# Kernel tuning notes

Measured on AMD Instinct MI355X. Metric: run time of the kernel, lower is better.

The kernel has to match this reference:

```python
import jax, jax.numpy as jnp
import numpy as np

N_NODES = 100000
N_EDGES = 1000000
NFEAT = 64
NHID = 64
NCLASS = 10
DROPOUT = 0.3
PAE_HID = 128  # hidden width of PAE in HOGCN/EV-GCN
EPS_BN = 1e-5
EPS_COS = 1e-8


def setup_inputs() -> dict:
    key = jax.random.key(0)
    ks = jax.random.split(key, 16)
    def w(k, shape, fan_in):
        return jax.random.normal(k, shape, dtype=jnp.float32) * (1.0 / np.sqrt(fan_in))
    inp = {
        "x": jax.random.normal(ks[0], (N_NODES, NFEAT), dtype=jnp.float32),
        "edge_index": jax.random.randint(ks[1], (2, N_EDGES), 0, N_NODES, dtype=jnp.int32),
        "edgenet_input": jax.random.normal(ks[2], (N_EDGES, 4), dtype=jnp.float32),
        # PAE params: Linear(2,128) -> ReLU -> BN(128) -> Dropout -> Linear(128,128)
        "pae_w1": w(ks[3], (2, PAE_HID), 2),
        "pae_b1": jnp.zeros((PAE_HID,), jnp.float32),
        "pae_gamma": jnp.ones((PAE_HID,), jnp.float32),
        "pae_beta": jnp.zeros((PAE_HID,), jnp.float32),
        "pae_w2": w(ks[4], (PAE_HID, PAE_HID), PAE_HID),
        "pae_b2": jnp.zeros((PAE_HID,), jnp.float32),
        # GCNConv layers
        "conv1_w": w(ks[5], (NFEAT, NHID), NFEAT),
        "conv1_b": jnp.zeros((NHID,), jnp.float32),
        "conv2_w": w(ks[6], (NHID, NHID), NHID),
        "conv2_b": jnp.zeros((NHID,), jnp.float32),
        # MLP head
        "lin1_w": w(ks[7], (NHID, NHID // 2), NHID),
        "lin1_b": jnp.zeros((NHID // 2,), jnp.float32),
        "lin2_w": w(ks[8], (NHID // 2, NCLASS), NHID // 2),
        "lin2_b": jnp.zeros((NCLASS,), jnp.float32),
    }
    return inp


def _pae(edgenet_input, w1, b1, gamma, beta, w2, b2, key):
    # Split edge input into the two endpoint halves; run shared parser on both.
    d = edgenet_input.shape[1] // 2
    x12 = jnp.stack([edgenet_input[:, :d], edgenet_input[:, d:]], axis=0)  # [2, E, d]
    h = jax.nn.relu(x12 @ w1 + b1)  # [2, E, H]
    # BatchNorm1d (training mode): stats over the edge batch, per parser call
    mean = h.mean(axis=1, keepdims=True)
    var = h.var(axis=1, keepdims=True)
    h = (h - mean) * jax.lax.rsqrt(var + EPS_BN) * gamma + beta
    keep = jax.random.bernoulli(key, 1.0 - DROPOUT, h.shape)
    h = jnp.where(keep, h / (1.0 - DROPOUT), 0.0)
    h = h @ w2 + b2
    h1, h2 = h[0], h[1]
    n1 = jnp.maximum(jnp.linalg.norm(h1, axis=-1), EPS_COS)
    n2 = jnp.maximum(jnp.linalg.norm(h2, axis=-1), EPS_COS)
    cos = (h1 * h2).sum(-1) / (n1 * n2)
    return (cos + 1.0) * 0.5  # [E]


def _gcn_conv(x, row, col, ew, W, b, n):
    # PyG GCNConv: add self-loops (weight 1), symmetric normalization, then
    # gather-scale-scatter aggregation of linearly transformed features.
    xw = x @ W  # [N, out]
    sl = jnp.arange(n, dtype=row.dtype)
    row_f = jnp.concatenate([row, sl])
    col_f = jnp.concatenate([col, sl])
    ew_f = jnp.concatenate([ew, jnp.ones((n,), ew.dtype)])
    deg = jax.ops.segment_sum(ew_f, col_f, num_segments=n)
    dinv = jnp.where(deg > 0, jax.lax.rsqrt(jnp.maximum(deg, 1e-12)), 0.0)
    norm = dinv[row_f] * ew_f * dinv[col_f]  # [E+N]
    msgs = norm[:, None] * xw[row_f]  # irregular gather + scale
    out = jax.ops.segment_sum(msgs, col_f, num_segments=n)  # scatter-add
    return out + b


def reference(x, edge_index, edgenet_input,
              pae_w1, pae_b1, pae_gamma, pae_beta, pae_w2, pae_b2,
              conv1_w, conv1_b, conv2_w, conv2_b,
              lin1_w, lin1_b, lin2_w, lin2_b):
    n = x.shape[0]
    row, col = edge_index[0], edge_index[1]
    k_pae, k_head = jax.random.split(jax.random.key(42))
    edge_weight = _pae(edgenet_input, pae_w1, pae_b1, pae_gamma, pae_beta,
                       pae_w2, pae_b2, k_pae)
    h = jax.nn.relu(_gcn_conv(x, row, col, edge_weight, conv1_w, conv1_b, n))
    h = jax.nn.relu(_gcn_conv(h, row, col, edge_weight, conv2_w, conv2_b, n))
    h = jax.nn.relu(h @ lin1_w + lin1_b)
    keep = jax.random.bernoulli(k_head, 1.0 - DROPOUT, h.shape)
    h = jnp.where(keep, h / (1.0 - DROPOUT), 0.0)
    out = h @ lin2_w + lin2_b
    return out
```

## Files before the change

kernel.cpp:

```cpp
#include <hip/hip_runtime.h>
#include <stdint.h>


#define NN 100000
#define NE 1000000
#define INV_KEEP (1.0f/0.7f)
#define KEEP_THR 3006477312u

#define BN_BLOCKS   1000
#define HIST_BLOCKS 3907
#define PAE_BLOCKS  31250
#define XW1_BLOCKS  1563
#define MEGA_GROUPS 782
#define MEGA_BLOCKS (MEGA_GROUPS * 47)

typedef short bf16x8 __attribute__((ext_vector_type(8)));
typedef float f32x4  __attribute__((ext_vector_type(4)));
typedef uint32_t u32x4 __attribute__((ext_vector_type(4)));

__host__ __device__ constexpr uint32_t rotl32c(uint32_t x, int r) {
  return (x << r) | (x >> (32 - r));
}

struct TFK { uint32_t a, b; };
__host__ __device__ constexpr TFK tf_const(uint32_t k0, uint32_t k1,
                                           uint32_t x0, uint32_t x1) {
  uint32_t k2 = k0 ^ k1 ^ 0x1BD11BDAu;
  x0 += k0; x1 += k1;
#define TFC_R(r) { x0 += x1; x1 = rotl32c(x1, (r)); x1 ^= x0; }
  TFC_R(13) TFC_R(15) TFC_R(26) TFC_R(6)   x0 += k1; x1 += k2 + 1u;
  TFC_R(17) TFC_R(29) TFC_R(16) TFC_R(24)  x0 += k2; x1 += k0 + 2u;
  TFC_R(13) TFC_R(15) TFC_R(26) TFC_R(6)   x0 += k0; x1 += k1 + 3u;
  TFC_R(17) TFC_R(29) TFC_R(16) TFC_R(24)  x0 += k1; x1 += k2 + 4u;
  TFC_R(13) TFC_R(15) TFC_R(26) TFC_R(6)   x0 += k2; x1 += k0 + 5u;
#undef TFC_R
  return TFK{x0, x1};
}

constexpr TFK KP = tf_const(0u, 42u, 0u, 0u);
constexpr TFK KH = tf_const(0u, 42u, 0u, 1u);

template <uint32_t K0, uint32_t K1>
__device__ __forceinline__ uint32_t tf_bits(uint32_t idx) {
  constexpr uint32_t K2 = K0 ^ K1 ^ 0x1BD11BDAu;
  uint32_t x0 = K0;
  uint32_t x1 = idx + K1;
#define TF_R(r) { x0 += x1; \
    x1 = __builtin_amdgcn_alignbit(x1, x1, 32u - (r)) ^ x0; }
  TF_R(13) TF_R(15) TF_R(26) TF_R(6)   x0 += K1; x1 += K2 + 1u;
  TF_R(17) TF_R(29) TF_R(16) TF_R(24)  x0 += K2; x1 += K0 + 2u;
  TF_R(13) TF_R(15) TF_R(26) TF_R(6)   x0 += K0; x1 += K1 + 3u;
  TF_R(17) TF_R(29) TF_R(16) TF_R(24)  x0 += K1; x1 += K2 + 4u;
  TF_R(13) TF_R(15) TF_R(26) TF_R(6)   x0 += K2; x1 += K0 + 5u;
#undef TF_R
  return x0 ^ x1;
}

__device__ __forceinline__ uint16_t f2bf(float f) {
  uint32_t u = __float_as_uint(f);
  return (uint16_t)((u + 0x7FFFu + ((u >> 16) & 1u)) >> 16);
}

__device__ __forceinline__ float bf2f(uint16_t u) {
  return __uint_as_float((uint32_t)u << 16);
}

__global__ __launch_bounds__(256) void phase1(const float* __restrict__ edgenet,
                                              const float* __restrict__ w1,
                                              const float* __restrict__ b1,
                                              const int* __restrict__ colp,
                                              float* __restrict__ sums,
                                              int* __restrict__ cnt) {
  int b = blockIdx.x;
  int t = threadIdx.x;
  if (b < BN_BLOCKS) {
    int c = t & 127, g = t >> 7;
    float wA = w1[c], wB = w1[128 + c], bb = b1[c];
    const float4* ed4 = (const float4*)edgenet;
    int e0 = b * 1000;
    float s0 = 0.f, q0 = 0.f, s1 = 0.f, q1 = 0.f;
#pragma unroll 4
    for (int e = g; e < 1000; e += 2) {
      float4 x = ed4[e0 + e];
      float h = fmaxf(fmaf(x.y, wB, fmaf(x.x, wA, bb)), 0.f);
      s0 += h; q0 = fmaf(h, h, q0);
      h = fmaxf(fmaf(x.w, wB, fmaf(x.z, wA, bb)), 0.f);
      s1 += h; q1 = fmaf(h, h, q1);
    }
    atomicAdd(&sums[c], s0);
    atomicAdd(&sums[256 + c], q0);
    atomicAdd(&sums[128 + c], s1);
    atomicAdd(&sums[384 + c], q1);
  } else {
    int e = (b - BN_BLOCKS) * 256 + t;
    if (e < NE) atomicAdd(&cnt[colp[e]], 1);
  }
}

__global__ __launch_bounds__(256) void csr_scanA(const int* __restrict__ cnt,
                                                 int* __restrict__ ptr,
                                                 int* __restrict__ bsum) {
  __shared__ int sh[256];
  int t = threadIdx.x;
  int i = blockIdx.x * 256 + t;
  int x = (i < NN) ? cnt[i] : 0;
  sh[t] = x;
  __syncthreads();
  for (int o = 1; o < 256; o <<= 1) {
    int v = (t >= o) ? sh[t - o] : 0;
    __syncthreads();
    sh[t] += v;
    __syncthreads();
  }
  if (i < NN) ptr[i] = sh[t] - x;
  if (t == 255) bsum[blockIdx.x] = sh[255];
}

__global__ __launch_bounds__(512) void scanAddPrep(const int* __restrict__ bsum,
                                                   int* __restrict__ ptr,
                                                   int* __restrict__ fill,
                                                   const float* __restrict__ sums,
                                                   const float* __restrict__ w1,
                                                   const float* __restrict__ b1,
                                                   const float* __restrict__ gamma,
                                                   const float* __restrict__ beta,
                                                   const float* __restrict__ w2,
                                                   float* __restrict__ prm,
                                                   uint32_t* __restrict__ w2t) {
  int b = blockIdx.x;
  int t = threadIdx.x;
  if (b < 391) {
    __shared__ int sh[512];
    int x = (t < 391) ? bsum[t] : 0;
    sh[t] = x;
    __syncthreads();
    for (int o = 1; o < 512; o <<= 1) {
      int v = (t >= o) ? sh[t - o] : 0;
      __syncthreads();
      sh[t] += v;
      __syncthreads();
    }
    int excl = (b == 0) ? 0 : sh[b - 1];
    if (t < 256) {
      int i = b * 256 + t;
      if (i < NN) {
        int v = ptr[i] + excl;
        ptr[i] = v;
        fill[i] = v;
        if (i == NN - 1) ptr[NN] = NE;
      }
    }
  } else if (b < 407) {
    int i = (b - 391) * 512 + t;
    int n = i >> 6, kp = i & 63;
    float f0 = w2[(2 * kp) * 128 + n];
    float f1 = w2[(2 * kp + 1) * 128 + n];
    w2t[i] = (uint32_t)f2bf(f0) | ((uint32_t)f2bf(f1) << 16);
  } else if (t < 256) {
    int c = t & 127;
    const float invE = 1.0f / (float)NE;
    float mean = sums[t] * invE;
    float var = fmaxf(sums[256 + t] * invE - mean * mean, 0.f);
    float rstd = rsqrtf(var + 1e-5f);
    float a = gamma[c] * rstd;
    prm[384 + t] = a * INV_KEEP;
    prm[640 + t] = (beta[c] - mean * a) * INV_KEEP;
    if (t < 128) { prm[t] = w1[t]; prm[128 + t] = w1[128 + t]; prm[256 + t] = b1[t]; }
  }
}

__global__ __launch_bounds__(256, 6) void mega(const float* __restrict__ edgenet,
                                               const float* __restrict__ prm_g,
                                               const uint32_t* __restrict__ w2t,
                                               const float* __restrict__ b2,
                                               const int* __restrict__ rowp,
                                               const int* __restrict__ colp,
                                               float* __restrict__ ew_out,
                                               float* __restrict__ deg,
                                               int* __restrict__ fill,
                                               int2* __restrict__ epk,
                                               const float* __restrict__ x,
                                               const float* __restrict__ c1w,
                                               uint16_t* __restrict__ xw1) {
  __shared__ __align__(16) uint8_t smem[17408];
  int b = blockIdx.x;
  int t = threadIdx.x;
  int g = b % 47, u = b / 47;

  if (g < 40) {
    int blk = u * 40 + g;
    if (blk >= PAE_BLOCKS) return;
    float* prm = (float*)smem;
    float* b2s = (float*)(smem + 3584);
    int e0 = blk * 32;
    for (int i = t; i < 896; i += 256) prm[i] = prm_g[i];
    if (t < 128) b2s[t] = b2[t];
    __syncthreads();

    int lane = t & 63, w = t >> 6;
    int cl = lane & 15, quad = lane >> 4;
    int quad8 = quad * 8;
    int row = 16 * w + cl;
    int el = row >> 1, s = row & 1;
    int so = s << 7;
    float2 xv = *(const float2*)&edgenet[(size_t)(e0 + el) * 4 + 2 * s];
    uint32_t rowbase = (uint32_t)(e0 + el) * 128u + (s ? 128000000u : 0u);
    const u32x4* w2v = (const u32x4*)w2t;

    f32x4 acc[8];
#pragma unroll
    for (int nt = 0; nt < 8; ++nt) acc[nt] = (f32x4){0.f, 0.f, 0.f, 0.f};

#pragma unroll 1
    for (int kt = 0; kt < 4; ++kt) {
      u32x4 bfv[8];
#pragma unroll
      for (int nt = 0; nt < 8; ++nt)
        bfv[nt] = w2v[(nt * 16 + cl) * 16 + kt * 4 + quad];

      int c0 = kt * 32 + quad8;
      uint32_t idxbase = rowbase + (uint32_t)c0;
      float wa[8], wb[8], bb[8], ak[8], bk[8];
      *(float4*)&wa[0] = *(const float4*)&prm[c0];
      *(float4*)&wa[4] = *(const float4*)&prm[c0 + 4];
      *(float4*)&wb[0] = *(const float4*)&prm[128 + c0];
      *(float4*)&wb[4] = *(const float4*)&prm[132 + c0];
      *(float4*)&bb[0] = *(const float4*)&prm[256 + c0];
      *(float4*)&bb[4] = *(const float4*)&prm[260 + c0];
      *(float4*)&ak[0] = *(const float4*)&prm[384 + so + c0];
      *(float4*)&ak[4] = *(const float4*)&prm[388 + so + c0];
      *(float4*)&bk[0] = *(const float4*)&prm[640 + so + c0];
      *(float4*)&bk[4] = *(const float4*)&prm[644 + so + c0];
      uint32_t pk[4];
#pragma unroll
      for (int jp = 0; jp < 4; ++jp) {
        uint32_t uu[2];
#pragma unroll
        for (int q = 0; q < 2; ++q) {
          int j = 2 * jp + q;
          float h = fmaxf(fmaf(xv.y, wb[j], fmaf(xv.x, wa[j], bb[j])), 0.f);
          float hn = fmaf(h, ak[j], bk[j]);
          uint32_t bits = tf_bits<KP.a, KP.b>(idxbase + (uint32_t)j);
          float hd = (bits < KEEP_THR) ? hn : 0.f;
          uu[q] = __float_as_uint(hd) + 0x8000u;
        }
        pk[jp] = __builtin_amdgcn_perm(uu[1], uu[0], 0x07060302u);
      }
      u32x4 pkv = {pk[0], pk[1], pk[2], pk[3]};
      bf16x8 afr = __builtin_bit_cast(bf16x8, pkv);
#pragma unroll
      for (int nt = 0; nt < 8; ++nt) {
        bf16x8 bfr = __builtin_bit_cast(bf16x8, bfv[nt]);
        acc[nt] = __builtin_amdgcn_mfma_f32_16x16x32_bf16(afr, bfr, acc[nt], 0, 0, 0);
      }
    }

    float p11[2] = {0.f, 0.f}, p22[2] = {0.f, 0.f}, p12[2] = {0.f, 0.f};
#pragma unroll
    for (int nt = 0; nt < 8; ++nt) {
      float bv = b2s[nt * 16 + cl];
#pragma unroll
      for (int uq = 0; uq < 2; ++uq) {
        float v1 = acc[nt][2 * uq] + bv;
        float v2 = acc[nt][2 * uq + 1] + bv;
        p11[uq] = fmaf(v1, v1, p11[uq]);
        p22[uq] = fmaf(v2, v2, p22[uq]);
        p12[uq] = fmaf(v1, v2, p12[uq]);
      }
    }
#pragma unroll
    for (int uq = 0; uq < 2; ++uq) {
      float a = p11[uq], bq = p22[uq], d = p12[uq];
      for (int off = 1; off < 16; off <<= 1) {
        a += __shfl_xor(a, off, 64);
        bq += __shfl_xor(bq, off, 64);
        d += __shfl_xor(d, off, 64);
      }
      if (cl == 0) {
        int e = e0 + 8 * w + 2 * quad + uq;
        float n1 = fmaxf(sqrtf(a), 1e-8f);
        float n2 = fmaxf(sqrtf(bq), 1e-8f);
        float ew = (d / (n1 * n2) + 1.f) * 0.5f;
        ew_out[e] = ew;
        atomicAdd(&deg[colp[e]], ew);
      }
    }
  } else if (g < 45) {
    int blk = u * 5 + (g - 40);
    if (blk >= HIST_BLOCKS) return;
    int e = blk * 256 + t;
    if (e < NE) {
      int r = rowp[e];
      int p = atomicAdd(&fill[colp[e]], 1);
      epk[p] = make_int2(r, e);
    }
  } else {
    int blk = u * 2 + (g - 45);
    if (blk >= XW1_BLOCKS) return;
    float* InT = (float*)smem;
    int v0 = blk * 64;
    for (int i = t; i < 4096; i += 256) {
      int v = i >> 6, k = i & 63;
      int vv = min(v0 + v, NN - 1);
      InT[k * 68 + v] = x[(size_t)vv * 64 + k];
    }
    __syncthreads();
    int tx = t & 15, ty = t >> 4;
    float acc[4][4];
#pragma unroll
    for (int i = 0; i < 4; ++i)
#pragma unroll
      for (int j = 0; j < 4; ++j) acc[i][j] = 0.f;
#pragma unroll 4
    for (int k = 0; k < 64; ++k) {
      float4 av = *(const float4*)&InT[k * 68 + 4 * ty];
      float4 bv = *(const float4*)&c1w[k * 64 + 4 * tx];
      float a4[4] = {av.x, av.y, av.z, av.w};
      float b4[4] = {bv.x, bv.y, bv.z, bv.w};
#pragma unroll
      for (int i = 0; i < 4; ++i)
#pragma unroll
        for (int j = 0; j < 4; ++j) acc[i][j] = fmaf(a4[i], b4[j], acc[i][j]);
    }
    for (int i = 0; i < 4; ++i) {
      int v = v0 + 4 * ty + i;
      if (v < NN) {
        uint32_t p0 = __builtin_amdgcn_perm(__float_as_uint(acc[i][1]) + 0x8000u,
                                            __float_as_uint(acc[i][0]) + 0x8000u,
                                            0x07060302u);
        uint32_t p1 = __builtin_amdgcn_perm(__float_as_uint(acc[i][3]) + 0x8000u,
                                            __float_as_uint(acc[i][2]) + 0x8000u,
                                            0x07060302u);
        *(uint2*)&xw1[(size_t)v * 64 + 4 * tx] = make_uint2(p0, p1);
      }
    }
  }
}

__global__ void csr_coef(int2* __restrict__ epk, const float* __restrict__ ew,
                         const float* __restrict__ deg) {
  int p = (blockIdx.x * 256 + threadIdx.x) * 2;
  if (p < NE) {
    int2 a = epk[p];
    int2 b = epk[p + 1];
    float da = deg[a.x], db = deg[b.x];
    float ea = ew[a.y], eb = ew[b.y];
    epk[p]     = make_int2(a.x, __float_as_int(rsqrtf(da + 1.0f) * ea));
    epk[p + 1] = make_int2(b.x, __float_as_int(rsqrtf(db + 1.0f) * eb));
  }
}

__global__ __launch_bounds__(256) void conv1g(const int* __restrict__ ptr,
                                              const int2* __restrict__ epk,
                                              const float* __restrict__ deg,
                                              const uint16_t* __restrict__ xw,
                                              const float* __restrict__ bias,
                                              uint16_t* __restrict__ h1) {
  int t = threadIdx.x;
  int v = blockIdx.x * 4 + (t >> 6);
  int c = t & 63;
  int p = ptr[v], end = ptr[v + 1];
  float acc = 0.f;
  while (p + 4 <= end) {
    int2 e0 = epk[p], e1 = epk[p + 1], e2 = epk[p + 2], e3 = epk[p + 3];
    float x0 = bf2f(xw[(size_t)e0.x * 64 + c]);
    float x1 = bf2f(xw[(size_t)e1.x * 64 + c]);
    float x2 = bf2f(xw[(size_t)e2.x * 64 + c]);
    float x3 = bf2f(xw[(size_t)e3.x * 64 + c]);
    acc = fmaf(__int_as_float(e0.y), x0, acc);
    acc = fmaf(__int_as_float(e1.y), x1, acc);
    acc = fmaf(__int_as_float(e2.y), x2, acc);
    acc = fmaf(__int_as_float(e3.y), x3, acc);
    p += 4;
  }
  if (p + 2 <= end) {
    int2 e0 = epk[p], e1 = epk[p + 1];
    float x0 = bf2f(xw[(size_t)e0.x * 64 + c]);
    float x1 = bf2f(xw[(size_t)e1.x * 64 + c]);
    acc = fmaf(__int_as_float(e0.y), x0, acc);
    acc = fmaf(__int_as_float(e1.y), x1, acc);
    p += 2;
  }
  if (p < end) {
    int2 a = epk[p];
    acc = fmaf(__int_as_float(a.y), bf2f(xw[(size_t)a.x * 64 + c]), acc);
  }
  float dv = rsqrtf(deg[v] + 1.0f);
  float val = fmaf(dv, acc, fmaf(dv * dv, bf2f(xw[(size_t)v * 64 + c]), bias[c]));
  h1[(size_t)v * 64 + c] = f2bf(fmaxf(val, 0.f));
}

__global__ __launch_bounds__(256) void conv2_head(const int* __restrict__ ptr,
                                                  const int2* __restrict__ epk,
                                                  const float* __restrict__ deg,
                                                  const uint16_t* __restrict__ h1,
                                                  const float* __restrict__ W,
                                                  const float* __restrict__ bias,
                                                  const float* __restrict__ l1w,
                                                  const float* __restrict__ l1b,
                                                  const float* __restrict__ l2w,
                                                  const float* __restrict__ l2b,
                                                  float* __restrict__ out) {
  __shared__ __align__(16) float T[16 * 68];
  __shared__ __align__(16) float H2[16 * 68];
  __shared__ float L2s[320];
  __shared__ float biass[64], l1bs[32], l2bs[16];
  int t = threadIdx.x;
  for (int i = t; i < 320; i += 256) L2s[i] = l2w[i];
  if (t < 64) biass[t] = bias[t];
  if (t < 32) l1bs[t] = l1b[t];
  if (t < 10) l2bs[t] = l2b[t];
  int w = t >> 6, c = t & 63;
  int v0 = blockIdx.x * 16;
#pragma unroll 1
  for (int i = 0; i < 4; ++i) {
    int n = 4 * w + i;
    int v = v0 + n;
    int p = ptr[v], end = ptr[v + 1];
    float acc = 0.f;
    while (p + 4 <= end) {
      int2 e0 = epk[p], e1 = epk[p + 1], e2 = epk[p + 2], e3 = epk[p + 3];
      float x0 = bf2f(h1[(size_t)e0.x * 64 + c]);
      float x1 = bf2f(h1[(size_t)e1.x * 64 + c]);
      float x2 = bf2f(h1[(size_t)e2.x * 64 + c]);
      float x3 = bf2f(h1[(size_t)e3.x * 64 + c]);
      acc = fmaf(__int_as_float(e0.y), x0, acc);
      acc = fmaf(__int_as_float(e1.y), x1, acc);
      acc = fmaf(__int_as_float(e2.y), x2, acc);
      acc = fmaf(__int_as_float(e3.y), x3, acc);
      p += 4;
    }
    if (p + 2 <= end) {
      int2 e0 = epk[p], e1 = epk[p + 1];
      float x0 = bf2f(h1[(size_t)e0.x * 64 + c]);
      float x1 = bf2f(h1[(size_t)e1.x * 64 + c]);
      acc = fmaf(__int_as_float(e0.y), x0, acc);
      acc = fmaf(__int_as_float(e1.y), x1, acc);
      p += 2;
    }
    if (p < end) {
      int2 a = epk[p];
      acc = fmaf(__int_as_float(a.y), bf2f(h1[(size_t)a.x * 64 + c]), acc);
    }
    float dv = rsqrtf(deg[v] + 1.0f);
    T[n * 68 + c] = fmaf(dv, acc, dv * dv * bf2f(h1[(size_t)v * 64 + c]));
  }
  __syncthreads();
  {
    int n = t >> 4, cq = (t & 15) * 4;
    float4 o = *(const float4*)&biass[cq];
#pragma unroll 4
    for (int k = 0; k < 64; ++k) {
      float a = T[n * 68 + k];
      float4 wv = *(const float4*)&W[k * 64 + cq];
      o.x = fmaf(a, wv.x, o.x);
      o.y = fmaf(a, wv.y, o.y);
      o.z = fmaf(a, wv.z, o.z);
      o.w = fmaf(a, wv.w, o.w);
    }
    o.x = fmaxf(o.x, 0.f); o.y = fmaxf(o.y, 0.f);
    o.z = fmaxf(o.z, 0.f); o.w = fmaxf(o.w, 0.f);
    __syncthreads();
    *(float4*)&H2[n * 68 + cq] = o;
  }
  __syncthreads();
  {
    int n = t >> 4, j0 = t & 15;
#pragma unroll
    for (int jj = 0; jj < 2; ++jj) {
      int j = j0 + 16 * jj;
      float m = l1bs[j];
#pragma unroll 4
      for (int k = 0; k < 64; ++k) m = fmaf(H2[n * 68 + k], l1w[k * 32 + j], m);
      m = fmaxf(m, 0.f);
      uint32_t idx = (uint32_t)(v0 + n) * 32u + (uint32_t)j;
      bool kp = tf_bits<KH.a, KH.b>(idx) < KEEP_THR;
      T[n * 33 + j] = kp ? m * INV_KEEP : 0.f;
    }
  }
  __syncthreads();
  if (t < 160) {
    int n = t / 10, f = t % 10;
    float s = l2bs[f];
#pragma unroll
    for (int j = 0; j < 32; ++j) s = fmaf(T[n * 33 + j], L2s[j * 10 + f], s);
    out[(size_t)(v0 + n) * 10 + f] = s;
  }
}

extern "C" void kernel_launch(void* const* d_in, const int* in_sizes, int n_in,
                              void* d_out, int out_size, void* d_ws, size_t ws_size,
                              hipStream_t stream) {
  const float* x       = (const float*)d_in[0];
  const int*   ei      = (const int*)d_in[1];
  const float* edgenet = (const float*)d_in[2];
  const float* pw1     = (const float*)d_in[3];
  const float* pb1     = (const float*)d_in[4];
  const float* pgamma  = (const float*)d_in[5];
  const float* pbeta   = (const float*)d_in[6];
  const float* pw2     = (const float*)d_in[7];
  const float* pb2     = (const float*)d_in[8];
  const float* c1w     = (const float*)d_in[9];
  const float* c1b     = (const float*)d_in[10];
  const float* c2w     = (const float*)d_in[11];
  const float* c2b     = (const float*)d_in[12];
  const float* l1w     = (const float*)d_in[13];
  const float* l1b     = (const float*)d_in[14];
  const float* l2w     = (const float*)d_in[15];
  const float* l2b     = (const float*)d_in[16];
  float* out = (float*)d_out;

  const int* rowp = ei;
  const int* colp = ei + NE;

  float* wsf      = (float*)d_ws;
  float* bn_sums  = wsf;
  float* DEG      = wsf + 512;
  int*   CNT      = (int*)(wsf + 512 + NN);
  float* EW       = wsf + 512 + 2 * NN;
  int*   PTR      = (int*)(EW + NE);
  int*   FILL     = PTR + NN + 1;
  int*   BSUM     = FILL + NN;
  uint32_t* W2T   = (uint32_t*)(BSUM + 512);
  float* PRM      = (float*)(W2T + 8192);
  int2*  EPK      = (int2*)(PRM + 898);
  uint16_t* XW1   = (uint16_t*)(EPK + NE);
  uint16_t* H1    = XW1 + (size_t)NN * 64;

  hipMemsetAsync(bn_sums, 0, (512 + 2 * NN) * sizeof(float), stream);

  phase1<<<BN_BLOCKS + HIST_BLOCKS, 256, 0, stream>>>(edgenet, pw1, pb1, colp,
                                                      bn_sums, CNT);
  csr_scanA<<<391, 256, 0, stream>>>(CNT, PTR, BSUM);
  scanAddPrep<<<408, 512, 0, stream>>>(BSUM, PTR, FILL, bn_sums, pw1, pb1,
                                       pgamma, pbeta, pw2, PRM, W2T);

  mega<<<MEGA_BLOCKS, 256, 0, stream>>>(edgenet, PRM, W2T, pb2, rowp, colp,
                                        EW, DEG, FILL, EPK, x, c1w, XW1);

  csr_coef<<<(NE / 2 + 255) / 256, 256, 0, stream>>>(EPK, EW, DEG);

  conv1g<<<NN / 4, 256, 0, stream>>>(PTR, EPK, DEG, XW1, c1b, H1);
  conv2_head<<<NN / 16, 256, 0, stream>>>(PTR, EPK, DEG, H1, c2w, c2b,
                                          l1w, l1b, l2w, l2b, out);
}
```

Baseline: 976.6 us.

## Gather packed bf16 pairs per lane in GCN aggregation; vectorize degree histogram

Result: faster. 946.1 us, median of 2 (-3.1%).

```diff
diff --git a/kernel.cpp b/kernel.cpp
--- a/kernel.cpp
+++ b/kernel.cpp
@@ -8,7 +8,8 @@
 #define KEEP_THR 3006477312u
 
 #define BN_BLOCKS   1000
-#define HIST_BLOCKS 3907
+#define HIST_BLOCKS 977
+#define FILL_BLOCKS 3907
 #define PAE_BLOCKS  31250
 #define XW1_BLOCKS  1563
 #define MEGA_GROUPS 782
@@ -61,8 +62,15 @@
   return (uint16_t)((u + 0x7FFFu + ((u >> 16) & 1u)) >> 16);
 }
 
-__device__ __forceinline__ float bf2f(uint16_t u) {
-  return __uint_as_float((uint32_t)u << 16);
+__device__ __forceinline__ float bflo(uint32_t u) {
+  return __uint_as_float(u << 16);
+}
+__device__ __forceinline__ float bfhi(uint32_t u) {
+  return __uint_as_float(u & 0xFFFF0000u);
+}
+__device__ __forceinline__ uint32_t packbf(float a, float b) {
+  return __builtin_amdgcn_perm(__float_as_uint(b) + 0x8000u,
+                               __float_as_uint(a) + 0x8000u, 0x07060302u);
 }
 
 __global__ __launch_bounds__(256) void phase1(const float* __restrict__ edgenet,
@@ -92,8 +100,14 @@
     atomicAdd(&sums[128 + c], s1);
     atomicAdd(&sums[384 + c], q1);
   } else {
-    int e = (b - BN_BLOCKS) * 256 + t;
-    if (e < NE) atomicAdd(&cnt[colp[e]], 1);
+    int e = ((b - BN_BLOCKS) * 256 + t) * 4;
+    if (e < NE) {
+      int4 cc = *(const int4*)&colp[e];
+      atomicAdd(&cnt[cc.x], 1);
+      atomicAdd(&cnt[cc.y], 1);
+      atomicAdd(&cnt[cc.z], 1);
+      atomicAdd(&cnt[cc.w], 1);
+    }
   }
 }
 
@@ -181,7 +195,7 @@
                                                int2* __restrict__ epk,
                                                const float* __restrict__ x,
                                                const float* __restrict__ c1w,
-                                               uint16_t* __restrict__ xw1) {
+                                               uint32_t* __restrict__ xw1) {
   __shared__ __align__(16) uint8_t smem[17408];
   int b = blockIdx.x;
   int t = threadIdx.x;
@@ -287,7 +301,7 @@
     }
   } else if (g < 45) {
     int blk = u * 5 + (g - 40);
-    if (blk >= HIST_BLOCKS) return;
+    if (blk >= FILL_BLOCKS) return;
     int e = blk * 256 + t;
     if (e < NE) {
       int r = rowp[e];
@@ -325,13 +339,9 @@
     for (int i = 0; i < 4; ++i) {
       int v = v0 + 4 * ty + i;
       if (v < NN) {
-        uint32_t p0 = __builtin_amdgcn_perm(__float_as_uint(acc[i][1]) + 0x8000u,
-                                            __float_as_uint(acc[i][0]) + 0x8000u,
-                                            0x07060302u);
-        uint32_t p1 = __builtin_amdgcn_perm(__float_as_uint(acc[i][3]) + 0x8000u,
-                                            __float_as_uint(acc[i][2]) + 0x8000u,
-                                            0x07060302u);
-        *(uint2*)&xw1[(size_t)v * 64 + 4 * tx] = make_uint2(p0, p1);
+        uint32_t p0 = packbf(acc[i][0], acc[i][1]);
+        uint32_t p1 = packbf(acc[i][2], acc[i][3]);
+        *(uint2*)&xw1[(size_t)v * 32 + 2 * tx] = make_uint2(p0, p1);
       }
     }
   }
@@ -353,47 +363,56 @@
 __global__ __launch_bounds__(256) void conv1g(const int* __restrict__ ptr,
                                               const int2* __restrict__ epk,
                                               const float* __restrict__ deg,
-                                              const uint16_t* __restrict__ xw,
+                                              const uint32_t* __restrict__ xw,
                                               const float* __restrict__ bias,
-                                              uint16_t* __restrict__ h1) {
+                                              uint32_t* __restrict__ h1) {
   int t = threadIdx.x;
-  int v = blockIdx.x * 4 + (t >> 6);
-  int c = t & 63;
+  int v = blockIdx.x * 8 + (t >> 5);
+  int chp = t & 31;
   int p = ptr[v], end = ptr[v + 1];
-  float acc = 0.f;
+  float a0 = 0.f, a1 = 0.f;
   while (p + 4 <= end) {
     int2 e0 = epk[p], e1 = epk[p + 1], e2 = epk[p + 2], e3 = epk[p + 3];
-    float x0 = bf2f(xw[(size_t)e0.x * 64 + c]);
-    float x1 = bf2f(xw[(size_t)e1.x * 64 + c]);
-    float x2 = bf2f(xw[(size_t)e2.x * 64 + c]);
-    float x3 = bf2f(xw[(size_t)e3.x * 64 + c]);
-    acc = fmaf(__int_as_float(e0.y), x0, acc);
-    acc = fmaf(__int_as_float(e1.y), x1, acc);
-    acc = fmaf(__int_as_float(e2.y), x2, acc);
-    acc = fmaf(__int_as_float(e3.y), x3, acc);
+    uint32_t r0 = xw[(size_t)e0.x * 32 + chp];
+    uint32_t r1 = xw[(size_t)e1.x * 32 + chp];
+    uint32_t r2 = xw[(size_t)e2.x * 32 + chp];
+    uint32_t r3 = xw[(size_t)e3.x * 32 + chp];
+    float c0 = __int_as_float(e0.y), c1 = __int_as_float(e1.y);
+    float c2 = __int_as_float(e2.y), c3 = __int_as_float(e3.y);
+    a0 = fmaf(c0, bflo(r0), a0); a1 = fmaf(c0, bfhi(r0), a1);
+    a0 = fmaf(c1, bflo(r1), a0); a1 = fmaf(c1, bfhi(r1), a1);
+    a0 = fmaf(c2, bflo(r2), a0); a1 = fmaf(c2, bfhi(r2), a1);
+    a0 = fmaf(c3, bflo(r3), a0); a1 = fmaf(c3, bfhi(r3), a1);
     p += 4;
   }
   if (p + 2 <= end) {
     int2 e0 = epk[p], e1 = epk[p + 1];
-    float x0 = bf2f(xw[(size_t)e0.x * 64 + c]);
-    float x1 = bf2f(xw[(size_t)e1.x * 64 + c]);
-    acc = fmaf(__int_as_float(e0.y), x0, acc);
-    acc = fmaf(__int_as_float(e1.y), x1, acc);
+    uint32_t r0 = xw[(size_t)e0.x * 32 + chp];
+    uint32_t r1 = xw[(size_t)e1.x * 32 + chp];
+    float c0 = __int_as_float(e0.y), c1 = __int_as_float(e1.y);
+    a0 = fmaf(c0, bflo(r0), a0); a1 = fmaf(c0, bfhi(r0), a1);
+    a0 = fmaf(c1, bflo(r1), a0); a1 = fmaf(c1, bfhi(r1), a1);
     p += 2;
   }
   if (p < end) {
-    int2 a = epk[p];
-    acc = fmaf(__int_as_float(a.y), bf2f(xw[(size_t)a.x * 64 + c]), acc);
+    int2 e0 = epk[p];
+    uint32_t r0 = xw[(size_t)e0.x * 32 + chp];
+    float c0 = __int_as_float(e0.y);
+    a0 = fmaf(c0, bflo(r0), a0); a1 = fmaf(c0, bfhi(r0), a1);
   }
   float dv = rsqrtf(deg[v] + 1.0f);
-  float val = fmaf(dv, acc, fmaf(dv * dv, bf2f(xw[(size_t)v * 64 + c]), bias[c]));
-  h1[(size_t)v * 64 + c] = f2bf(fmaxf(val, 0.f));
+  float dv2 = dv * dv;
+  uint32_t sf = xw[(size_t)v * 32 + chp];
+  float2 bv = *(const float2*)&bias[2 * chp];
+  float v0 = fmaf(dv, a0, fmaf(dv2, bflo(sf), bv.x));
+  float v1 = fmaf(dv, a1, fmaf(dv2, bfhi(sf), bv.y));
+  h1[(size_t)v * 32 + chp] = packbf(fmaxf(v0, 0.f), fmaxf(v1, 0.f));
 }
 
 __global__ __launch_bounds__(256) void conv2_head(const int* __restrict__ ptr,
                                                   const int2* __restrict__ epk,
                                                   const float* __restrict__ deg,
-                                                  const uint16_t* __restrict__ h1,
+                                                  const uint32_t* __restrict__ h1,
                                                   const float* __restrict__ W,
                                                   const float* __restrict__ bias,
                                                   const float* __restrict__ l1w,
@@ -410,40 +429,48 @@
   if (t < 64) biass[t] = bias[t];
   if (t < 32) l1bs[t] = l1b[t];
   if (t < 10) l2bs[t] = l2b[t];
-  int w = t >> 6, c = t & 63;
+  int w = t >> 6, h = (t >> 5) & 1, chp = t & 31;
   int v0 = blockIdx.x * 16;
 #pragma unroll 1
-  for (int i = 0; i < 4; ++i) {
-    int n = 4 * w + i;
+  for (int i = 0; i < 2; ++i) {
+    int n = 4 * w + 2 * i + h;
     int v = v0 + n;
     int p = ptr[v], end = ptr[v + 1];
-    float acc = 0.f;
+    float a0 = 0.f, a1 = 0.f;
     while (p + 4 <= end) {
       int2 e0 = epk[p], e1 = epk[p + 1], e2 = epk[p + 2], e3 = epk[p + 3];
-      float x0 = bf2f(h1[(size_t)e0.x * 64 + c]);
-      float x1 = bf2f(h1[(size_t)e1.x * 64 + c]);
-      float x2 = bf2f(h1[(size_t)e2.x * 64 + c]);
-      float x3 = bf2f(h1[(size_t)e3.x * 64 + c]);
-      acc = fmaf(__int_as_float(e0.y), x0, acc);
-      acc = fmaf(__int_as_float(e1.y), x1, acc);
-      acc = fmaf(__int_as_float(e2.y), x2, acc);
-      acc = fmaf(__int_as_float(e3.y), x3, acc);
+      uint32_t r0 = h1[(size_t)e0.x * 32 + chp];
+      uint32_t r1 = h1[(size_t)e1.x * 32 + chp];
+      uint32_t r2 = h1[(size_t)e2.x * 32 + chp];
+      uint32_t r3 = h1[(size_t)e3.x * 32 + chp];
+      float c0 = __int_as_float(e0.y), c1 = __int_as_float(e1.y);
+      float c2 = __int_as_float(e2.y), c3 = __int_as_float(e3.y);
+      a0 = fmaf(c0, bflo(r0), a0); a1 = fmaf(c0, bfhi(r0), a1);
+      a0 = fmaf(c1, bflo(r1), a0); a1 = fmaf(c1, bfhi(r1), a1);
+      a0 = fmaf(c2, bflo(r2), a0); a1 = fmaf(c2, bfhi(r2), a1);
+      a0 = fmaf(c3, bflo(r3), a0); a1 = fmaf(c3, bfhi(r3), a1);
       p += 4;
     }
     if (p + 2 <= end) {
       int2 e0 = epk[p], e1 = epk[p + 1];
-      float x0 = bf2f(h1[(size_t)e0.x * 64 + c]);
-      float x1 = bf2f(h1[(size_t)e1.x * 64 + c]);
-      acc = fmaf(__int_as_float(e0.y), x0, acc);
-      acc = fmaf(__int_as_float(e1.y), x1, acc);
+      uint32_t r0 = h1[(size_t)e0.x * 32 + chp];
+      uint32_t r1 = h1[(size_t)e1.x * 32 + chp];
+      float c0 = __int_as_float(e0.y), c1 = __int_as_float(e1.y);
+      a0 = fmaf(c0, bflo(r0), a0); a1 = fmaf(c0, bfhi(r0), a1);
+      a0 = fmaf(c1, bflo(r1), a0); a1 = fmaf(c1, bfhi(r1), a1);
       p += 2;
     }
     if (p < end) {
-      int2 a = epk[p];
-      acc = fmaf(__int_as_float(a.y), bf2f(h1[(size_t)a.x * 64 + c]), acc);
+      int2 e0 = epk[p];
+      uint32_t r0 = h1[(size_t)e0.x * 32 + chp];
+      float c0 = __int_as_float(e0.y);
+      a0 = fmaf(c0, bflo(r0), a0); a1 = fmaf(c0, bfhi(r0), a1);
     }
     float dv = rsqrtf(deg[v] + 1.0f);
-    T[n * 68 + c] = fmaf(dv, acc, dv * dv * bf2f(h1[(size_t)v * 64 + c]));
+    float dv2 = dv * dv;
+    uint32_t sf = h1[(size_t)v * 32 + chp];
+    *(float2*)&T[n * 68 + 2 * chp] =
+        make_float2(fmaf(dv, a0, dv2 * bflo(sf)), fmaf(dv, a1, dv2 * bfhi(sf)));
   }
   __syncthreads();
   {
@@ -524,8 +551,8 @@
   uint32_t* W2T   = (uint32_t*)(BSUM + 512);
   float* PRM      = (float*)(W2T + 8192);
   int2*  EPK      = (int2*)(PRM + 898);
-  uint16_t* XW1   = (uint16_t*)(EPK + NE);
-  uint16_t* H1    = XW1 + (size_t)NN * 64;
+  uint32_t* XW1   = (uint32_t*)(EPK + NE);
+  uint32_t* H1    = XW1 + (size_t)NN * 32;
 
   hipMemsetAsync(bn_sums, 0, (512 + 2 * NN) * sizeof(float), stream);
 
@@ -540,7 +567,7 @@
 
   csr_coef<<<(NE / 2 + 255) / 256, 256, 0, stream>>>(EPK, EW, DEG);
 
-  conv1g<<<NN / 4, 256, 0, stream>>>(PTR, EPK, DEG, XW1, c1b, H1);
+  conv1g<<<NN / 8, 256, 0, stream>>>(PTR, EPK, DEG, XW1, c1b, H1);
   conv2_head<<<NN / 16, 256, 0, stream>>>(PTR, EPK, DEG, H1, c2w, c2b,
                                           l1w, l1b, l2w, l2b, out);
 }
```
